# Kernel optimization log

Measured on AMD Instinct MI355X. Metric: run time of the kernel, lower is better.

The kernel has to match this reference:

```python
import jax, jax.numpy as jnp
import numpy as np

EPS = 1e-8  # torch F.cosine_similarity denominator clamp


def setup_inputs() -> dict:
    key = jax.random.key(0)
    k1, k2 = jax.random.split(key)
    N, D = 8192, 256
    return {
        "output1": jax.random.normal(k1, (N, D), dtype=jnp.float32),
        "output2": jax.random.normal(k2, (N, D), dtype=jnp.float32),
    }


def reference(output1, output2):
    N = output2.shape[0]
    # cosine similarity matrix via normalize + GEMM, with torch's eps clamp
    n1 = jnp.linalg.norm(output1, axis=-1, keepdims=True)  # [N,1]
    n2 = jnp.linalg.norm(output2, axis=-1, keepdims=True)  # [N,1]
    dots = output1 @ output2.T  # [N,N]
    denom = jnp.maximum(n1 * n2.T, EPS)
    cos = dots / denom
    # subtract tiny diagonal as in original
    cos = cos - jnp.eye(N, dtype=cos.dtype) * 1e-12
    # cross entropy with labels = arange(N)
    logZ = jax.nn.logsumexp(cos, axis=-1)  # [N]
    diag = jnp.diagonal(cos)  # logits at true label i
    loss = jnp.mean(logZ - diag)
    return loss
```

## Files before the change

kernel.cpp:

```cpp
#include <hip/hip_runtime.h>
#include <hip/hip_bf16.h>

#define N 8192
#define D 256
#define SP 8
#define NCHK 16
#define LOG2E 1.44269504088896f

typedef int   i32x4 __attribute__((ext_vector_type(4)));
typedef int   i32x8 __attribute__((ext_vector_type(8)));
typedef float f32x4 __attribute__((ext_vector_type(4)));

static __device__ __forceinline__ void gll16(const void* g, void* l) {
    __builtin_amdgcn_global_load_lds(
        (const __attribute__((address_space(1))) void*)g,
        (__attribute__((address_space(3))) void*)l, 16, 0, 0);
}

#define WAIT_VM0  asm volatile("s_waitcnt vmcnt(0)" ::: "memory")
#define WAIT_LG0  asm volatile("s_waitcnt lgkmcnt(0)" ::: "memory")
#define SBAR      __builtin_amdgcn_s_barrier()
#define SCHED0    __builtin_amdgcn_sched_barrier(0)

__global__ __launch_bounds__(256) void conv_k(const float* __restrict__ o1,
                                              const float* __restrict__ o2,
                                              unsigned char* __restrict__ a8,
                                              unsigned char* __restrict__ b8,
                                              float* __restrict__ diag) {
    const int wid = threadIdx.x >> 6, lane = threadIdx.x & 63;
    const int r = blockIdx.x * 4 + wid;
    const float4* p1 = (const float4*)(o1 + (size_t)r * D);
    const float4* p2 = (const float4*)(o2 + (size_t)r * D);
    float4 v1 = p1[lane], v2 = p2[lane];
    float s1 = v1.x*v1.x + v1.y*v1.y + v1.z*v1.z + v1.w*v1.w;
    float s2 = v2.x*v2.x + v2.y*v2.y + v2.z*v2.z + v2.w*v2.w;
    float sd = v1.x*v2.x + v1.y*v2.y + v1.z*v2.z + v1.w*v2.w;
    #pragma unroll
    for (int m = 1; m < 64; m <<= 1) {
        s1 += __shfl_xor(s1, m);
        s2 += __shfl_xor(s2, m);
        sd += __shfl_xor(sd, m);
    }
    float i1 = 1.0f / sqrtf(s1);
    float i2 = 1.0f / sqrtf(s2);
    if (lane == 0) diag[r] = sd * i1 * i2;

    float a_sc = i1 * LOG2E;
    {
        int pa = __builtin_amdgcn_cvt_pk_fp8_f32(v1.x * a_sc, v1.y * a_sc, 0, false);
        pa     = __builtin_amdgcn_cvt_pk_fp8_f32(v1.z * a_sc, v1.w * a_sc, pa, true);
        *(int*)(a8 + (size_t)r * 256 + lane * 4) = pa;
    }
    {
        int pb = __builtin_amdgcn_cvt_pk_fp8_f32(v2.x * i2, v2.y * i2, 0, false);
        pb     = __builtin_amdgcn_cvt_pk_fp8_f32(v2.z * i2, v2.w * i2, pb, true);
        int c  = lane >> 2;
        int cs = c ^ (r & 15);
        *(int*)(b8 + (size_t)r * 256 + cs * 16 + (lane & 3) * 4) = pb;
    }
}

__global__ __launch_bounds__(256, 2) void gemm11(const unsigned char* __restrict__ a8,
                                                 const unsigned char* __restrict__ b8,
                                                 float* __restrict__ s_part) {
    __shared__ __align__(16) unsigned char bls[2][16384];
    __shared__ float red[2][128];

    const int tid = threadIdx.x;
    const int lane = tid & 63, wid = tid >> 6;
    const int wr = wid >> 1, wc = wid & 1;
    const int l15 = lane & 15, lk = lane >> 4;
    const int bid = blockIdx.x;
    const int panel = bid & 7, rb = bid >> 3;

    const unsigned char* aG = a8 + (size_t)rb * (128 * 256);
    const unsigned char* bG = b8 + (size_t)panel * ((size_t)1024 * 256);

    i32x8 af[4][2];
    #pragma unroll
    for (int mr = 0; mr < 4; ++mr)
        #pragma unroll
        for (int kh = 0; kh < 2; ++kh)
            af[mr][kh] = *(const i32x8*)(aG + (size_t)(wr * 64 + mr * 16 + l15) * 256
                                            + kh * 128 + lk * 32);

    #pragma unroll
    for (int it = 0; it < 4; ++it) {
        int x = it * 4096 + tid * 16;
        gll16(bG + x, &bls[0][x]);
    }

    float srow[4][4];
    #pragma unroll
    for (int mr = 0; mr < 4; ++mr)
        #pragma unroll
        for (int rg = 0; rg < 4; ++rg) srow[mr][rg] = 0.f;

    int cur = 0;

    #pragma unroll 1
    for (int p = 0; p < NCHK; ++p) {
        WAIT_VM0;
        SCHED0;
        SBAR;

        if (p < NCHK - 1) {
            const unsigned char* src = bG + (size_t)(p + 1) * 16384;
            unsigned char* dst = bls[cur ^ 1];
            #pragma unroll
            for (int it = 0; it < 4; ++it) {
                int x = it * 4096 + tid * 16;
                gll16(src + x, dst + x);
            }
        }

        f32x4 acc[4][2];
        #pragma unroll
        for (int mr = 0; mr < 4; ++mr)
            #pragma unroll
            for (int nc = 0; nc < 2; ++nc)
                acc[mr][nc] = (f32x4){0.f, 0.f, 0.f, 0.f};

        const unsigned char* cb = bls[cur];

        __builtin_amdgcn_s_setprio(1);
        #pragma unroll
        for (int kh = 0; kh < 2; ++kh) {
            i32x8 bb[2];
            #pragma unroll
            for (int nc = 0; nc < 2; ++nc) {
                const int col = wc * 32 + nc * 16 + l15;
                const int c0  = kh * 8 + lk * 2;
                const int cs0 = c0 ^ l15;
                i32x4 lo = *(const i32x4*)(cb + col * 256 + cs0 * 16);
                i32x4 hi = *(const i32x4*)(cb + col * 256 + (cs0 ^ 1) * 16);
                i32x8 b;
                b[0] = lo[0]; b[1] = lo[1]; b[2] = lo[2]; b[3] = lo[3];
                b[4] = hi[0]; b[5] = hi[1]; b[6] = hi[2]; b[7] = hi[3];
                bb[nc] = b;
            }
            #pragma unroll
            for (int nc = 0; nc < 2; ++nc)
                #pragma unroll
                for (int mr = 0; mr < 4; ++mr)
                    acc[mr][nc] = __builtin_amdgcn_mfma_scale_f32_16x16x128_f8f6f4(
                        af[mr][kh], bb[nc], acc[mr][nc],
                        0, 0,
                        0, 0x7F,
                        0, 0x7F);
        }
        __builtin_amdgcn_s_setprio(0);
        WAIT_LG0;
        SCHED0;

        #pragma unroll
        for (int mr = 0; mr < 4; ++mr)
            #pragma unroll
            for (int rg = 0; rg < 4; ++rg)
                srow[mr][rg] += exp2f(acc[mr][0][rg]) + exp2f(acc[mr][1][rg]);

        cur ^= 1;
    }

    #pragma unroll
    for (int mr = 0; mr < 4; ++mr)
        #pragma unroll
        for (int rg = 0; rg < 4; ++rg) {
            float v = srow[mr][rg];
            v += __shfl_xor(v, 1);
            v += __shfl_xor(v, 2);
            v += __shfl_xor(v, 4);
            v += __shfl_xor(v, 8);
            srow[mr][rg] = v;
        }
    if (l15 == 0) {
        #pragma unroll
        for (int mr = 0; mr < 4; ++mr)
            #pragma unroll
            for (int rg = 0; rg < 4; ++rg)
                red[wc][wr * 64 + mr * 16 + lk * 4 + rg] = srow[mr][rg];
    }
    __syncthreads();
    if (tid < 128) {
        s_part[(size_t)panel * N + rb * 128 + tid] = red[0][tid] + red[1][tid];
    }
}

__global__ __launch_bounds__(128) void rowloss3(const float* __restrict__ s_part,
                                                const float* __restrict__ diag,
                                                float* __restrict__ partial) {
    const int t = threadIdx.x, rb = blockIdx.x;
    float s = 0.f;
    #pragma unroll
    for (int sp = 0; sp < SP; ++sp)
        s += s_part[(size_t)sp * N + rb * 128 + t];
    float loss = logf(s) - diag[rb * 128 + t];
    #pragma unroll
    for (int m = 1; m < 64; m <<= 1) loss += __shfl_xor(loss, m);
    __shared__ float redl[2];
    if ((t & 63) == 0) redl[t >> 6] = loss;
    __syncthreads();
    if (t == 0) partial[rb] = redl[0] + redl[1];
}

__global__ __launch_bounds__(64) void final_k(const float* __restrict__ partial,
                                              float* __restrict__ out) {
    const int t = threadIdx.x;
    float v = partial[t];
    #pragma unroll
    for (int m = 1; m < 64; m <<= 1) v += __shfl_xor(v, m);
    if (t == 0) out[0] = v / (float)N;
}

extern "C" void kernel_launch(void* const* d_in, const int* in_sizes, int n_in,
                              void* d_out, int out_size, void* d_ws, size_t ws_size,
                              hipStream_t stream) {
    const float* o1 = (const float*)d_in[0];
    const float* o2 = (const float*)d_in[1];

    unsigned char* w = (unsigned char*)d_ws;
    unsigned char* a8 = w;
    unsigned char* b8 = w + (size_t)2 * 1024 * 1024;
    float* diag    = (float*)(w + (size_t)4 * 1024 * 1024);
    float* s_part  = diag + N;
    float* partial = s_part + (size_t)SP * N;

    conv_k<<<N / 4, 256, 0, stream>>>(o1, o2, a8, b8, diag);
    gemm11<<<512, 256, 0, stream>>>(a8, b8, s_part);
    rowloss3<<<N / 128, 128, 0, stream>>>(s_part, diag, partial);
    final_k<<<1, 64, 0, stream>>>(partial, (float*)d_out);
}
```

Measured before the change: 46.41 us.

## Load B operands directly from global into registers, dropping LDS staging

The GEMM kernel no longer stages B panels in shared memory through global_load_lds with barriers. Each wave now loads its B fragments straight from global memory into registers, using a two-deep register ping-pong to overlap loads with MFMA and exp work. The conversion kernel stops writing the XOR swizzle, since the fragments are no longer read from LDS. This removes the barriers and LDS traffic, but each wave now fetches B from L2/global on its own, which duplicates reads across the two wave rows and raises register pressure.

Result: slower. 52.26 us (+12.6%).

```diff
diff --git a/kernel.cpp b/kernel.cpp
--- a/kernel.cpp
+++ b/kernel.cpp
@@ -7,20 +7,8 @@
 #define NCHK 16
 #define LOG2E 1.44269504088896f
 
-typedef int   i32x4 __attribute__((ext_vector_type(4)));
 typedef int   i32x8 __attribute__((ext_vector_type(8)));
 typedef float f32x4 __attribute__((ext_vector_type(4)));
-
-static __device__ __forceinline__ void gll16(const void* g, void* l) {
-    __builtin_amdgcn_global_load_lds(
-        (const __attribute__((address_space(1))) void*)g,
-        (__attribute__((address_space(3))) void*)l, 16, 0, 0);
-}
-
-#define WAIT_VM0  asm volatile("s_waitcnt vmcnt(0)" ::: "memory")
-#define WAIT_LG0  asm volatile("s_waitcnt lgkmcnt(0)" ::: "memory")
-#define SBAR      __builtin_amdgcn_s_barrier()
-#define SCHED0    __builtin_amdgcn_sched_barrier(0)
 
 __global__ __launch_bounds__(256) void conv_k(const float* __restrict__ o1,
                                               const float* __restrict__ o2,
@@ -54,16 +42,13 @@
     {
         int pb = __builtin_amdgcn_cvt_pk_fp8_f32(v2.x * i2, v2.y * i2, 0, false);
         pb     = __builtin_amdgcn_cvt_pk_fp8_f32(v2.z * i2, v2.w * i2, pb, true);
-        int c  = lane >> 2;
-        int cs = c ^ (r & 15);
-        *(int*)(b8 + (size_t)r * 256 + cs * 16 + (lane & 3) * 4) = pb;
+        *(int*)(b8 + (size_t)r * 256 + lane * 4) = pb;
     }
 }
 
-__global__ __launch_bounds__(256, 2) void gemm11(const unsigned char* __restrict__ a8,
+__global__ __launch_bounds__(256, 2) void gemm12(const unsigned char* __restrict__ a8,
                                                  const unsigned char* __restrict__ b8,
                                                  float* __restrict__ s_part) {
-    __shared__ __align__(16) unsigned char bls[2][16384];
     __shared__ float red[2][128];
 
     const int tid = threadIdx.x;
@@ -74,7 +59,7 @@
     const int panel = bid & 7, rb = bid >> 3;
 
     const unsigned char* aG = a8 + (size_t)rb * (128 * 256);
-    const unsigned char* bG = b8 + (size_t)panel * ((size_t)1024 * 256);
+    const unsigned char* bW = b8 + (size_t)(panel * 1024 + wc * 32 + l15) * 256 + lk * 32;
 
     i32x8 af[4][2];
     #pragma unroll
@@ -84,83 +69,60 @@
             af[mr][kh] = *(const i32x8*)(aG + (size_t)(wr * 64 + mr * 16 + l15) * 256
                                             + kh * 128 + lk * 32);
 
-    #pragma unroll
-    for (int it = 0; it < 4; ++it) {
-        int x = it * 4096 + tid * 16;
-        gll16(bG + x, &bls[0][x]);
-    }
-
     float srow[4][4];
     #pragma unroll
     for (int mr = 0; mr < 4; ++mr)
         #pragma unroll
         for (int rg = 0; rg < 4; ++rg) srow[mr][rg] = 0.f;
 
-    int cur = 0;
+#define LOADB(DST, P)                                                           \
+    {                                                                           \
+        _Pragma("unroll")                                                       \
+        for (int kh_ = 0; kh_ < 2; ++kh_)                                       \
+            _Pragma("unroll")                                                   \
+            for (int nc_ = 0; nc_ < 2; ++nc_)                                   \
+                DST[kh_][nc_] = *(const i32x8*)(bW + (size_t)((P) * 64 + nc_ * 16) * 256 \
+                                                   + kh_ * 128);                \
+    }
+
+#define COMPUTE(BB)                                                             \
+    {                                                                           \
+        f32x4 acc[4][2];                                                        \
+        _Pragma("unroll")                                                       \
+        for (int mr_ = 0; mr_ < 4; ++mr_)                                       \
+            _Pragma("unroll")                                                   \
+            for (int nc_ = 0; nc_ < 2; ++nc_)                                   \
+                acc[mr_][nc_] = (f32x4){0.f, 0.f, 0.f, 0.f};                    \
+        __builtin_amdgcn_s_setprio(1);                                          \
+        _Pragma("unroll")                                                       \
+        for (int kh_ = 0; kh_ < 2; ++kh_)                                       \
+            _Pragma("unroll")                                                   \
+            for (int nc_ = 0; nc_ < 2; ++nc_)                                   \
+                _Pragma("unroll")                                               \
+                for (int mr_ = 0; mr_ < 4; ++mr_)                               \
+                    acc[mr_][nc_] = __builtin_amdgcn_mfma_scale_f32_16x16x128_f8f6f4( \
+                        af[mr_][kh_], BB[kh_][nc_], acc[mr_][nc_],              \
+                        0, 0, 0, 0x7F, 0, 0x7F);                                \
+        __builtin_amdgcn_s_setprio(0);                                          \
+        _Pragma("unroll")                                                       \
+        for (int mr_ = 0; mr_ < 4; ++mr_)                                       \
+            _Pragma("unroll")                                                   \
+            for (int rg_ = 0; rg_ < 4; ++rg_)                                   \
+                srow[mr_][rg_] += exp2f(acc[mr_][0][rg_]) + exp2f(acc[mr_][1][rg_]); \
+    }
+
+    i32x8 bbA[2][2], bbB[2][2];
+    LOADB(bbA, 0);
 
     #pragma unroll 1
-    for (int p = 0; p < NCHK; ++p) {
-        WAIT_VM0;
-        SCHED0;
-        SBAR;
-
-        if (p < NCHK - 1) {
-            const unsigned char* src = bG + (size_t)(p + 1) * 16384;
-            unsigned char* dst = bls[cur ^ 1];
-            #pragma unroll
-            for (int it = 0; it < 4; ++it) {
-                int x = it * 4096 + tid * 16;
-                gll16(src + x, dst + x);
-            }
-        }
-
-        f32x4 acc[4][2];
-        #pragma unroll
-        for (int mr = 0; mr < 4; ++mr)
-            #pragma unroll
-            for (int nc = 0; nc < 2; ++nc)
-                acc[mr][nc] = (f32x4){0.f, 0.f, 0.f, 0.f};
-
-        const unsigned char* cb = bls[cur];
-
-        __builtin_amdgcn_s_setprio(1);
-        #pragma unroll
-        for (int kh = 0; kh < 2; ++kh) {
-            i32x8 bb[2];
-            #pragma unroll
-            for (int nc = 0; nc < 2; ++nc) {
-                const int col = wc * 32 + nc * 16 + l15;
-                const int c0  = kh * 8 + lk * 2;
-                const int cs0 = c0 ^ l15;
-                i32x4 lo = *(const i32x4*)(cb + col * 256 + cs0 * 16);
-                i32x4 hi = *(const i32x4*)(cb + col * 256 + (cs0 ^ 1) * 16);
-                i32x8 b;
-                b[0] = lo[0]; b[1] = lo[1]; b[2] = lo[2]; b[3] = lo[3];
-                b[4] = hi[0]; b[5] = hi[1]; b[6] = hi[2]; b[7] = hi[3];
-                bb[nc] = b;
-            }
-            #pragma unroll
-            for (int nc = 0; nc < 2; ++nc)
-                #pragma unroll
-                for (int mr = 0; mr < 4; ++mr)
-                    acc[mr][nc] = __builtin_amdgcn_mfma_scale_f32_16x16x128_f8f6f4(
-                        af[mr][kh], bb[nc], acc[mr][nc],
-                        0, 0,
-                        0, 0x7F,
-                        0, 0x7F);
-        }
-        __builtin_amdgcn_s_setprio(0);
-        WAIT_LG0;
-        SCHED0;
-
-        #pragma unroll
-        for (int mr = 0; mr < 4; ++mr)
-            #pragma unroll
-            for (int rg = 0; rg < 4; ++rg)
-                srow[mr][rg] += exp2f(acc[mr][0][rg]) + exp2f(acc[mr][1][rg]);
-
-        cur ^= 1;
+    for (int p = 0; p < NCHK; p += 2) {
+        if (p + 1 < NCHK) LOADB(bbB, p + 1);
+        COMPUTE(bbA);
+        if (p + 2 < NCHK) LOADB(bbA, p + 2);
+        if (p + 1 < NCHK) COMPUTE(bbB);
     }
+#undef LOADB
+#undef COMPUTE
 
     #pragma unroll
     for (int mr = 0; mr < 4; ++mr)
@@ -226,7 +188,7 @@
     float* partial = s_part + (size_t)SP * N;
 
     conv_k<<<N / 4, 256, 0, stream>>>(o1, o2, a8, b8, diag);
-    gemm11<<<512, 256, 0, stream>>>(a8, b8, s_part);
+    gemm12<<<512, 256, 0, stream>>>(a8, b8, s_part);
     rowloss3<<<N / 128, 128, 0, stream>>>(s_part, diag, partial);
     final_k<<<1, 64, 0, stream>>>(partial, (float*)d_out);
 }
```
